# Optimization experiments

Hardware: AMD Instinct MI355X
Metric: run time of the kernel (lower is better)

## Reference

```python
import jax, jax.numpy as jnp
import numpy as np


def gin_layer(x, src, dst, ew, w1, b1, w2, b2):
    # message: gather source features, scale by edge weight  [E, d]
    msg = x[src] * ew[:, None]
    # scatter-add into destination nodes  [N, d]
    agg = jax.ops.segment_sum(msg, dst, num_segments=x.shape[0])
    # GIN update: (1 + eps) * x + aggregate, eps = 0 (default)
    h = agg + x
    # 2-layer MLP (Linear -> ReLU -> Linear, plain last layer)
    h = jax.nn.relu(h @ w1 + b1)
    return h @ w2 + b2


def setup_inputs() -> dict:
    key = jax.random.key(0)
    ks = jax.random.split(key, 16)
    N, E, D = 100000, 1000000, 64
    x = jax.random.normal(ks[0], (N, D), dtype=jnp.float32)
    edge_index = jax.random.randint(ks[1], (2, E), 0, N)
    edge_weight = jax.random.uniform(ks[2], (E,), dtype=jnp.float32)

    def lin(k, fi, fo):
        return jax.random.normal(k, (fi, fo), dtype=jnp.float32) * (1.0 / np.sqrt(fi))

    return {
        "x": x, "edge_index": edge_index, "edge_weight": edge_weight,
        "w11": lin(ks[3], 64, 64),  "b11": jnp.zeros(64, jnp.float32),
        "w12": lin(ks[4], 64, 64),  "b12": jnp.zeros(64, jnp.float32),
        "w21": lin(ks[5], 64, 128), "b21": jnp.zeros(128, jnp.float32),
        "w22": lin(ks[6], 128, 64), "b22": jnp.zeros(64, jnp.float32),
        "w31": lin(ks[7], 64, 64),  "b31": jnp.zeros(64, jnp.float32),
        "w32": lin(ks[8], 64, 64),  "b32": jnp.zeros(64, jnp.float32),
    }


def reference(x, edge_index, edge_weight,
              w11, b11, w12, b12,
              w21, b21, w22, b22,
              w31, b31, w32, b32):
    src, dst = edge_index[0], edge_index[1]
    # dropout is identity in eval mode
    h = gin_layer(x, src, dst, edge_weight, w11, b11, w12, b12)
    h = jax.nn.relu(h)
    h = gin_layer(h, src, dst, edge_weight, w21, b21, w22, b22)
    h = jax.nn.relu(h)
    h = gin_layer(h, src, dst, edge_weight, w31, b31, w32, b32)
    return h
```

## Files before the change

### kernel.cpp

```cpp
#include <hip/hip_runtime.h>
#include <math.h>


#define FEAT  64
#define BINW  128
#define BSH   7
#define NBLK  256
#define SRCB  25

typedef __attribute__((ext_vector_type(8))) short bfrag;
typedef __attribute__((ext_vector_type(4))) float ffrag;

__device__ __forceinline__ unsigned short f2bf_rne(float x) {
    union { float f; unsigned u; } v; v.f = x;
    unsigned r = (v.u + 0x7fffu + ((v.u >> 16) & 1u)) >> 16;
    return (unsigned short)r;
}
__device__ __forceinline__ float bf2f(unsigned short h) {
    union { unsigned u; float f; } v; v.u = ((unsigned)h) << 16;
    return v.f;
}

__device__ __forceinline__ void pack_one(const float* __restrict__ w,
                                         unsigned short* __restrict__ hi,
                                         unsigned short* __restrict__ lo,
                                         int K, int Hc, int i) {
    int KF = K >> 5;
    int j    = i & 7;
    int lane = (i >> 3) & 63;
    int fb   = i >> 9;
    int kf   = fb % KF;
    int cg   = fb / KF;
    int k    = kf * 32 + ((lane >> 4) << 3) + j;
    int col  = cg * 16 + (lane & 15);
    float x = w[k * Hc + col];
    unsigned short h = f2bf_rne(x);
    hi[i] = h;
    lo[i] = f2bf_rne(x - bf2f(h));
}

__global__ __launch_bounds__(256)
void k_pre(const float4* __restrict__ x4, ushort4* __restrict__ xb4,
           int n4, int gCvt,
           const int* __restrict__ dst, int* __restrict__ counts,
           int E, int NBINS,
           const float* w11, const float* w12, const float* w21,
           const float* w22, const float* w31, const float* w32,
           unsigned short* p11h, unsigned short* p11l,
           unsigned short* p12h, unsigned short* p12l,
           unsigned short* p21h, unsigned short* p21l,
           unsigned short* p22h, unsigned short* p22l,
           unsigned short* p31h, unsigned short* p31l,
           unsigned short* p32h, unsigned short* p32l) {
    __shared__ int h[1024];
    const int bb = blockIdx.x, tid = threadIdx.x;
    if (bb < gCvt) {
        int i = bb * 256 + tid;
        if (i < n4) {
            float4 v = x4[i];
            ushort4 o;
            o.x = f2bf_rne(v.x); o.y = f2bf_rne(v.y);
            o.z = f2bf_rne(v.z); o.w = f2bf_rne(v.w);
            xb4[i] = o;
        }
    } else if (bb < gCvt + NBLK) {
        const int b = bb - gCvt;
        for (int i = tid; i < NBINS; i += 256) h[i] = 0;
        __syncthreads();
        const int chunk = (E + NBLK - 1) / NBLK;
        const int ebeg = b * chunk;
        const int eend = (ebeg + chunk < E) ? ebeg + chunk : E;
        for (int e = ebeg + tid; e < eend; e += 256)
            atomicAdd(&h[dst[e] >> BSH], 1);
        __syncthreads();
        for (int i = tid; i < NBINS; i += 256)
            counts[i * NBLK + b] = h[i];
    } else {
        int i = (bb - gCvt - NBLK) * 256 + tid;
        if      (i <  4096) pack_one(w11, p11h, p11l,  64,  64, i);
        else if (i <  8192) pack_one(w12, p12h, p12l,  64,  64, i - 4096);
        else if (i < 16384) pack_one(w21, p21h, p21l,  64, 128, i - 8192);
        else if (i < 24576) pack_one(w22, p22h, p22l, 128,  64, i - 16384);
        else if (i < 28672) pack_one(w31, p31h, p31l,  64,  64, i - 24576);
        else                pack_one(w32, p32h, p32l,  64,  64, i - 28672);
    }
}

__global__ __launch_bounds__(256)
void k_scanA2(int* __restrict__ counts, int* __restrict__ bintotal,
              int* __restrict__ rowptr, int NBINS, int N, int E) {
    __shared__ int tmp[256];
    const int bin = blockIdx.x, tid = threadIdx.x;
    int c = counts[bin * NBLK + tid];
    tmp[tid] = c;
    __syncthreads();
    for (int off = 1; off < 256; off <<= 1) {
        int t = (tid >= off) ? tmp[tid - off] : 0;
        __syncthreads();
        tmp[tid] += t;
        __syncthreads();
    }
    counts[bin * NBLK + tid] = tmp[tid] - c;
    if (tid == 255) bintotal[bin] = tmp[255];
    if (bin == 0 && tid == 0) rowptr[N] = E;
}

__global__ __launch_bounds__(256)
void k_place2(const int* __restrict__ src, const int* __restrict__ dst,
              const float* __restrict__ ew, const int* __restrict__ counts,
              const int* __restrict__ bintotal, int* __restrict__ binstart,
              int2* __restrict__ binbuf, int E, int NBINS) {
    __shared__ int bs[1024];
    __shared__ int tmp[256];
    __shared__ int base[1024];
    const int b = blockIdx.x, tid = threadIdx.x;

    int v[4]; int s = 0;
#pragma unroll
    for (int j = 0; j < 4; ++j) {
        int idx = tid * 4 + j;
        v[j] = (idx < NBINS) ? bintotal[idx] : 0;
        s += v[j];
    }
    tmp[tid] = s;
    __syncthreads();
    for (int off = 1; off < 256; off <<= 1) {
        int t = (tid >= off) ? tmp[tid - off] : 0;
        __syncthreads();
        tmp[tid] += t;
        __syncthreads();
    }
    int run = tmp[tid] - s;
#pragma unroll
    for (int j = 0; j < 4; ++j) {
        bs[tid * 4 + j] = run;
        run += v[j];
    }
    __syncthreads();

    if (b == 0) {
        for (int i = tid; i < NBINS; i += 256) binstart[i] = bs[i];
        if (tid == 0) binstart[NBINS] = E;
    }

    for (int i = tid; i < NBINS; i += 256)
        base[i] = bs[i] + counts[i * NBLK + b];
    __syncthreads();

    const int chunk = (E + NBLK - 1) / NBLK;
    const int ebeg = b * chunk;
    const int eend = (ebeg + chunk < E) ? ebeg + chunk : E;
    for (int e = ebeg + tid; e < eend; e += 256) {
        int d = dst[e];
        int slot = atomicAdd(&base[d >> BSH], 1);
        int key = ((d & (BINW - 1)) << SRCB) | src[e];
        binbuf[slot] = make_int2(key, __float_as_int(ew[e]));
    }
}

__global__ __launch_bounds__(256)
void k_binsort(const int2* __restrict__ binbuf, const int* __restrict__ binstart,
               int* __restrict__ rowptr, int2* __restrict__ csr, int N) {
    __shared__ int cnt[BINW];
    __shared__ int cur[BINW];
    const int b    = blockIdx.x;
    const int base = binstart[b];
    const int ne   = binstart[b + 1] - base;
    const int tid  = threadIdx.x;

    if (tid < BINW) cnt[tid] = 0;
    __syncthreads();
    for (int i = tid; i < ne; i += 256)
        atomicAdd(&cnt[(binbuf[base + i].x >> SRCB) & (BINW - 1)], 1);
    __syncthreads();
    if (tid < BINW) cur[tid] = cnt[tid];
    __syncthreads();
    for (int off = 1; off < BINW; off <<= 1) {
        int v = (tid < BINW && tid >= off) ? cur[tid - off] : 0;
        __syncthreads();
        if (tid < BINW) cur[tid] += v;
        __syncthreads();
    }
    if (tid < BINW) {
        int ex = cur[tid] - cnt[tid];
        int node = b * BINW + tid;
        if (node < N) rowptr[node] = base + ex;
        cur[tid] = ex;
    }
    __syncthreads();
    for (int i = tid; i < ne; i += 256) {
        int2 e = binbuf[base + i];
        int dl = (e.x >> SRCB) & (BINW - 1);
        int r = atomicAdd(&cur[dl], 1);
        csr[base + r] = make_int2(e.x & ((1 << SRCB) - 1), e.y);
    }
}

template<int H, bool RELU_OUT, bool OUT_BF16>
__global__ __launch_bounds__(256)
void k_fused(const ushort* __restrict__ in, void* __restrict__ outv,
             const int* __restrict__ rowptr, const int2* __restrict__ csr,
             const unsigned short* __restrict__ w1h, const unsigned short* __restrict__ w1l,
             const float* __restrict__ b1,
             const unsigned short* __restrict__ w2h, const unsigned short* __restrict__ w2l,
             const float* __restrict__ b2, int N, int E) {
    constexpr int SH   = H + 4;
    constexpr int CG1  = H / 16;
    constexpr int CGH1 = CG1 / 4;
    constexpr int KF2  = H / 32;
    __shared__ float hs[16 * SH];

    const int t = threadIdx.x;
    const int wk = t >> 6, lane = t & 63;
    const int m = lane & 15, q = lane >> 4;
    const int tnode0 = blockIdx.x * 16;
    float* hw = hs;
    const ushort4* in4 = reinterpret_cast<const ushort4*>(in);

    int rp_l = 0;
    {
        int idx = tnode0 + wk * 4 + lane;
        if (lane <= 4) rp_l = rowptr[idx <= N ? idx : N];
    }

    int gnode = tnode0 + wk * 4 + q;
    int gnodeC = gnode < N ? gnode : N - 1;
    ushort4 xr = in4[(size_t)gnodeC * 16 + m];

    {
        const int nl  = wk * 4 + q;
        const int beg = __shfl(rp_l, q);
        const int end = __shfl(rp_l, q + 1);
        float4 acc = make_float4(0.f, 0.f, 0.f, 0.f);
        for (int p = beg; p < end; p += 16) {
            int   s[16];
            float w[16];
#pragma unroll
            for (int u = 0; u < 16; ++u) {
                int i = p + u;
                int2 ev = csr[i < E ? i : E - 1];
                s[u] = ev.x;
                w[u] = (i < end) ? __int_as_float(ev.y) : 0.f;
            }
            ushort4 v4[16];
#pragma unroll
            for (int u = 0; u < 16; ++u)
                v4[u] = in4[(unsigned)s[u] * 16u + m];
#pragma unroll
            for (int u = 0; u < 16; ++u) {
                acc.x = fmaf(w[u], bf2f(v4[u].x), acc.x);
                acc.y = fmaf(w[u], bf2f(v4[u].y), acc.y);
                acc.z = fmaf(w[u], bf2f(v4[u].z), acc.z);
                acc.w = fmaf(w[u], bf2f(v4[u].w), acc.w);
            }
        }
        acc.x += bf2f(xr.x); acc.y += bf2f(xr.y);
        acc.z += bf2f(xr.z); acc.w += bf2f(xr.w);
        *reinterpret_cast<float4*>(&hw[nl * SH + m * 4]) = acc;
    }
    __syncthreads();

    const bfrag* w1hp = reinterpret_cast<const bfrag*>(w1h);
    const bfrag* w1lp = reinterpret_cast<const bfrag*>(w1l);
    const bfrag* w2hp = reinterpret_cast<const bfrag*>(w2h);
    const bfrag* w2lp = reinterpret_cast<const bfrag*>(w2l);

    bfrag ah[2], al[2];
#pragma unroll
    for (int kf = 0; kf < 2; ++kf) {
        const float* base = &hw[m * SH + kf * 32 + q * 8];
        float4 u0 = *reinterpret_cast<const float4*>(base);
        float4 u1 = *reinterpret_cast<const float4*>(base + 4);
        float u[8] = {u0.x, u0.y, u0.z, u0.w, u1.x, u1.y, u1.z, u1.w};
#pragma unroll
        for (int j = 0; j < 8; ++j) {
            unsigned short hb = f2bf_rne(u[j]);
            ah[kf][j] = (short)hb;
            al[kf][j] = (short)f2bf_rne(u[j] - bf2f(hb));
        }
    }
    __syncthreads();

#pragma unroll
    for (int cgi = 0; cgi < CGH1; ++cgi) {
        const int cg = wk * CGH1 + cgi;
        ffrag c = {0.f, 0.f, 0.f, 0.f};
#pragma unroll
        for (int kf = 0; kf < 2; ++kf) {
            bfrag bh = w1hp[(cg * 2 + kf) * 64 + lane];
            bfrag bl = w1lp[(cg * 2 + kf) * 64 + lane];
            c = __builtin_amdgcn_mfma_f32_16x16x32_bf16(ah[kf], bh, c, 0, 0, 0);
            c = __builtin_amdgcn_mfma_f32_16x16x32_bf16(al[kf], bh, c, 0, 0, 0);
            c = __builtin_amdgcn_mfma_f32_16x16x32_bf16(ah[kf], bl, c, 0, 0, 0);
        }
        float bias = b1[cg * 16 + m];
#pragma unroll
        for (int r = 0; r < 4; ++r) {
            float hv = fmaxf(c[r] + bias, 0.f);
            hw[(q * 4 + r) * SH + cg * 16 + m] = hv;
        }
    }
    __syncthreads();

    bfrag gh[KF2], gl[KF2];
#pragma unroll
    for (int kf = 0; kf < KF2; ++kf) {
        const float* base = &hw[m * SH + kf * 32 + q * 8];
        float4 u0 = *reinterpret_cast<const float4*>(base);
        float4 u1 = *reinterpret_cast<const float4*>(base + 4);
        float u[8] = {u0.x, u0.y, u0.z, u0.w, u1.x, u1.y, u1.z, u1.w};
#pragma unroll
        for (int j = 0; j < 8; ++j) {
            unsigned short hb = f2bf_rne(u[j]);
            gh[kf][j] = (short)hb;
            gl[kf][j] = (short)f2bf_rne(u[j] - bf2f(hb));
        }
    }

    {
        const int cg = wk;
        ffrag c = {0.f, 0.f, 0.f, 0.f};
#pragma unroll
        for (int kf = 0; kf < KF2; ++kf) {
            bfrag bh = w2hp[(cg * KF2 + kf) * 64 + lane];
            bfrag bl = w2lp[(cg * KF2 + kf) * 64 + lane];
            c = __builtin_amdgcn_mfma_f32_16x16x32_bf16(gh[kf], bh, c, 0, 0, 0);
            c = __builtin_amdgcn_mfma_f32_16x16x32_bf16(gl[kf], bh, c, 0, 0, 0);
            c = __builtin_amdgcn_mfma_f32_16x16x32_bf16(gh[kf], bl, c, 0, 0, 0);
        }
        float bias = b2[cg * 16 + m];
#pragma unroll
        for (int r = 0; r < 4; ++r) {
            int nd = tnode0 + q * 4 + r;
            if (nd < N) {
                float v = c[r] + bias;
                if (RELU_OUT) v = fmaxf(v, 0.f);
                if (OUT_BF16)
                    ((unsigned short*)outv)[(size_t)nd * FEAT + cg * 16 + m] = f2bf_rne(v);
                else
                    ((float*)outv)[(size_t)nd * FEAT + cg * 16 + m] = v;
            }
        }
    }
}

extern "C" void kernel_launch(void* const* d_in, const int* in_sizes, int n_in,
                              void* d_out, int out_size, void* d_ws, size_t ws_size,
                              hipStream_t stream) {
    const float* x   = (const float*)d_in[0];
    const int*   ei  = (const int*)  d_in[1];
    const float* ew  = (const float*)d_in[2];
    const float* w11 = (const float*)d_in[3];
    const float* b11 = (const float*)d_in[4];
    const float* w12 = (const float*)d_in[5];
    const float* b12 = (const float*)d_in[6];
    const float* w21 = (const float*)d_in[7];
    const float* b21 = (const float*)d_in[8];
    const float* w22 = (const float*)d_in[9];
    const float* b22 = (const float*)d_in[10];
    const float* w31 = (const float*)d_in[11];
    const float* b31 = (const float*)d_in[12];
    const float* w32 = (const float*)d_in[13];
    const float* b32 = (const float*)d_in[14];

    const int N = in_sizes[0] / FEAT;
    const int E = in_sizes[2];
    const int* srci = ei;
    const int* dsti = ei + E;
    const int NBINS = (N + BINW - 1) >> BSH;

    unsigned short* xb0 = (unsigned short*)d_ws;
    unsigned short* xb1 = xb0 + (size_t)N * FEAT;
    int*   rowptr   = (int*)(xb1 + (size_t)N * FEAT);
    int*   counts   = rowptr + (N + 1);
    int*   bintotal = counts + NBINS * NBLK;
    int*   binstart = bintotal + NBINS;
    size_t a16 = ((size_t)(binstart + NBINS + 1) + 15) & ~(size_t)15;
    int2*  binbuf   = (int2*)a16;
    int2*  csr      = (int2*)(binbuf + E);
    size_t pk = (size_t)(csr + E);
    unsigned short* p11h = (unsigned short*)pk;
    unsigned short* p11l = p11h + 4096;
    unsigned short* p12h = p11l + 4096;
    unsigned short* p12l = p12h + 4096;
    unsigned short* p21h = p12l + 4096;
    unsigned short* p21l = p21h + 8192;
    unsigned short* p22h = p21l + 8192;
    unsigned short* p22l = p22h + 8192;
    unsigned short* p31h = p22l + 8192;
    unsigned short* p31l = p31h + 4096;
    unsigned short* p32h = p31l + 4096;
    unsigned short* p32l = p32h + 4096;
    float* outF = (float*)d_out;

    const int n4   = N * 16;
    const int gCvt = (n4 + 255) / 256;
    const int gMlp = (N + 15) / 16;
    const int gPre = gCvt + NBLK + 128;

    k_pre<<<gPre, 256, 0, stream>>>((const float4*)x, (ushort4*)xb0, n4, gCvt,
                                    dsti, counts, E, NBINS,
                                    w11, w12, w21, w22, w31, w32,
                                    p11h, p11l, p12h, p12l, p21h, p21l,
                                    p22h, p22l, p31h, p31l, p32h, p32l);
    k_scanA2 <<<NBINS, 256, 0, stream>>>(counts, bintotal, rowptr, NBINS, N, E);
    k_place2 <<<NBLK,  256, 0, stream>>>(srci, dsti, ew, counts, bintotal,
                                         binstart, binbuf, E, NBINS);
    k_binsort<<<NBINS, 256, 0, stream>>>(binbuf, binstart, rowptr, csr, N);

    k_fused<64,  true,  true ><<<gMlp, 256, 0, stream>>>(xb0, xb1, rowptr, csr,
                                                         p11h, p11l, b11, p12h, p12l, b12, N, E);
    k_fused<128, true,  true ><<<gMlp, 256, 0, stream>>>(xb1, xb0, rowptr, csr,
                                                         p21h, p21l, b21, p22h, p22l, b22, N, E);
    k_fused<64,  false, false><<<gMlp, 256, 0, stream>>>(xb0, outF, rowptr, csr,
                                                         p31h, p31l, b31, p32h, p32l, b32, N, E);
}
```

Baseline: 274.4 us.

## Pad per-node CSR segments to 16 edges and load edges as int4 pairs

```diff
diff --git a/kernel.cpp b/kernel.cpp
--- a/kernel.cpp
+++ b/kernel.cpp
@@ -7,6 +7,7 @@
 #define BSH   7
 #define NBLK  256
 #define SRCB  25
+#define PADSLACK 2048
 
 typedef __attribute__((ext_vector_type(8))) short bfrag;
 typedef __attribute__((ext_vector_type(4))) float ffrag;
@@ -87,8 +88,7 @@
 }
 
 __global__ __launch_bounds__(256)
-void k_scanA2(int* __restrict__ counts, int* __restrict__ bintotal,
-              int* __restrict__ rowptr, int NBINS, int N, int E) {
+void k_scanA2(int* __restrict__ counts, int* __restrict__ bintotal, int NBINS) {
     __shared__ int tmp[256];
     const int bin = blockIdx.x, tid = threadIdx.x;
     int c = counts[bin * NBLK + tid];
@@ -102,7 +102,6 @@
     }
     counts[bin * NBLK + tid] = tmp[tid] - c;
     if (tid == 255) bintotal[bin] = tmp[255];
-    if (bin == 0 && tid == 0) rowptr[N] = E;
 }
 
 __global__ __launch_bounds__(256)
@@ -160,20 +159,24 @@
 
 __global__ __launch_bounds__(256)
 void k_binsort(const int2* __restrict__ binbuf, const int* __restrict__ binstart,
-               int* __restrict__ rowptr, int2* __restrict__ csr, int N) {
+               int* __restrict__ pbeg, int* __restrict__ pend,
+               int2* __restrict__ csr_pad, int N) {
     __shared__ int cnt[BINW];
     __shared__ int cur[BINW];
+    __shared__ int pex[BINW];
     const int b    = blockIdx.x;
     const int base = binstart[b];
     const int ne   = binstart[b + 1] - base;
     const int tid  = threadIdx.x;
+    const int base_pad = ((base + 15) & ~15) + b * PADSLACK;
 
     if (tid < BINW) cnt[tid] = 0;
     __syncthreads();
     for (int i = tid; i < ne; i += 256)
         atomicAdd(&cnt[(binbuf[base + i].x >> SRCB) & (BINW - 1)], 1);
     __syncthreads();
-    if (tid < BINW) cur[tid] = cnt[tid];
+    int pc = 0;
+    if (tid < BINW) { pc = (cnt[tid] + 15) & ~15; cur[tid] = pc; }
     __syncthreads();
     for (int off = 1; off < BINW; off <<= 1) {
         int v = (tid < BINW && tid >= off) ? cur[tid - off] : 0;
@@ -182,28 +185,41 @@
         __syncthreads();
     }
     if (tid < BINW) {
-        int ex = cur[tid] - cnt[tid];
+        int ex = cur[tid] - pc;
+        pex[tid] = ex;
         int node = b * BINW + tid;
-        if (node < N) rowptr[node] = base + ex;
-        cur[tid] = ex;
+        if (node < N) {
+            pbeg[node] = base_pad + ex;
+            pend[node] = base_pad + ex + pc;
+        }
+        cur[tid] = 0;
     }
     __syncthreads();
     for (int i = tid; i < ne; i += 256) {
         int2 e = binbuf[base + i];
         int dl = (e.x >> SRCB) & (BINW - 1);
         int r = atomicAdd(&cur[dl], 1);
-        csr[base + r] = make_int2(e.x & ((1 << SRCB) - 1), e.y);
+        csr_pad[base_pad + pex[dl] + r] = make_int2(e.x & ((1 << SRCB) - 1), e.y);
+    }
+    __syncthreads();
+    if (tid < BINW) {
+        int c = cnt[tid];
+        int pcn = (c + 15) & ~15;
+        int o = base_pad + pex[tid];
+        for (int j = c; j < pcn; ++j)
+            csr_pad[o + j] = make_int2(0, 0);
     }
 }
 
 template<int H, bool RELU_OUT, bool OUT_BF16>
 __global__ __launch_bounds__(256)
 void k_fused(const ushort* __restrict__ in, void* __restrict__ outv,
-             const int* __restrict__ rowptr, const int2* __restrict__ csr,
+             const int* __restrict__ pbeg, const int* __restrict__ pend,
+             const int2* __restrict__ csr_pad,
              const unsigned short* __restrict__ w1h, const unsigned short* __restrict__ w1l,
              const float* __restrict__ b1,
              const unsigned short* __restrict__ w2h, const unsigned short* __restrict__ w2l,
-             const float* __restrict__ b2, int N, int E) {
+             const float* __restrict__ b2, int N) {
     constexpr int SH   = H + 4;
     constexpr int CG1  = H / 16;
     constexpr int CGH1 = CG1 / 4;
@@ -216,42 +232,39 @@
     const int tnode0 = blockIdx.x * 16;
     float* hw = hs;
     const ushort4* in4 = reinterpret_cast<const ushort4*>(in);
-
-    int rp_l = 0;
+    const int4* csr4 = reinterpret_cast<const int4*>(csr_pad);
+
+    const int gnode = tnode0 + wk * 4 + q;
+    const int beg = pbeg[gnode];
+    const int end = pend[gnode];
+    ushort4 xr = in4[(size_t)gnode * 16 + m];
+
     {
-        int idx = tnode0 + wk * 4 + lane;
-        if (lane <= 4) rp_l = rowptr[idx <= N ? idx : N];
-    }
-
-    int gnode = tnode0 + wk * 4 + q;
-    int gnodeC = gnode < N ? gnode : N - 1;
-    ushort4 xr = in4[(size_t)gnodeC * 16 + m];
-
-    {
-        const int nl  = wk * 4 + q;
-        const int beg = __shfl(rp_l, q);
-        const int end = __shfl(rp_l, q + 1);
+        const int nl = wk * 4 + q;
         float4 acc = make_float4(0.f, 0.f, 0.f, 0.f);
         for (int p = beg; p < end; p += 16) {
-            int   s[16];
-            float w[16];
-#pragma unroll
-            for (int u = 0; u < 16; ++u) {
-                int i = p + u;
-                int2 ev = csr[i < E ? i : E - 1];
-                s[u] = ev.x;
-                w[u] = (i < end) ? __int_as_float(ev.y) : 0.f;
+            int4 e2[8];
+#pragma unroll
+            for (int u = 0; u < 8; ++u)
+                e2[u] = csr4[(p >> 1) + u];
+            ushort4 v4[16];
+#pragma unroll
+            for (int u = 0; u < 8; ++u) {
+                v4[2*u]   = in4[(unsigned)e2[u].x * 16u + m];
+                v4[2*u+1] = in4[(unsigned)e2[u].z * 16u + m];
             }
-            ushort4 v4[16];
-#pragma unroll
-            for (int u = 0; u < 16; ++u)
-                v4[u] = in4[(unsigned)s[u] * 16u + m];
-#pragma unroll
-            for (int u = 0; u < 16; ++u) {
-                acc.x = fmaf(w[u], bf2f(v4[u].x), acc.x);
-                acc.y = fmaf(w[u], bf2f(v4[u].y), acc.y);
-                acc.z = fmaf(w[u], bf2f(v4[u].z), acc.z);
-                acc.w = fmaf(w[u], bf2f(v4[u].w), acc.w);
+#pragma unroll
+            for (int u = 0; u < 8; ++u) {
+                float w0 = __int_as_float(e2[u].y);
+                float w1 = __int_as_float(e2[u].w);
+                acc.x = fmaf(w0, bf2f(v4[2*u].x), acc.x);
+                acc.y = fmaf(w0, bf2f(v4[2*u].y), acc.y);
+                acc.z = fmaf(w0, bf2f(v4[2*u].z), acc.z);
+                acc.w = fmaf(w0, bf2f(v4[2*u].w), acc.w);
+                acc.x = fmaf(w1, bf2f(v4[2*u+1].x), acc.x);
+                acc.y = fmaf(w1, bf2f(v4[2*u+1].y), acc.y);
+                acc.z = fmaf(w1, bf2f(v4[2*u+1].z), acc.z);
+                acc.w = fmaf(w1, bf2f(v4[2*u+1].w), acc.w);
             }
         }
         acc.x += bf2f(xr.x); acc.y += bf2f(xr.y);
@@ -281,6 +294,7 @@
     }
     __syncthreads();
 
+    __builtin_amdgcn_s_setprio(1);
 #pragma unroll
     for (int cgi = 0; cgi < CGH1; ++cgi) {
         const int cg = wk * CGH1 + cgi;
@@ -300,6 +314,7 @@
             hw[(q * 4 + r) * SH + cg * 16 + m] = hv;
         }
     }
+    __builtin_amdgcn_s_setprio(0);
     __syncthreads();
 
     bfrag gh[KF2], gl[KF2];
@@ -320,6 +335,7 @@
     {
         const int cg = wk;
         ffrag c = {0.f, 0.f, 0.f, 0.f};
+        __builtin_amdgcn_s_setprio(1);
 #pragma unroll
         for (int kf = 0; kf < KF2; ++kf) {
             bfrag bh = w2hp[(cg * KF2 + kf) * 64 + lane];
@@ -328,6 +344,7 @@
             c = __builtin_amdgcn_mfma_f32_16x16x32_bf16(gl[kf], bh, c, 0, 0, 0);
             c = __builtin_amdgcn_mfma_f32_16x16x32_bf16(gh[kf], bl, c, 0, 0, 0);
         }
+        __builtin_amdgcn_s_setprio(0);
         float bias = b2[cg * 16 + m];
 #pragma unroll
         for (int r = 0; r < 4; ++r) {
@@ -371,14 +388,15 @@
 
     unsigned short* xb0 = (unsigned short*)d_ws;
     unsigned short* xb1 = xb0 + (size_t)N * FEAT;
-    int*   rowptr   = (int*)(xb1 + (size_t)N * FEAT);
-    int*   counts   = rowptr + (N + 1);
+    int*   pbeg     = (int*)(xb1 + (size_t)N * FEAT);
+    int*   pend     = pbeg + N;
+    int*   counts   = pend + N;
     int*   bintotal = counts + NBINS * NBLK;
     int*   binstart = bintotal + NBINS;
     size_t a16 = ((size_t)(binstart + NBINS + 1) + 15) & ~(size_t)15;
     int2*  binbuf   = (int2*)a16;
-    int2*  csr      = (int2*)(binbuf + E);
-    size_t pk = (size_t)(csr + E);
+    int2*  csr_pad  = (int2*)(binbuf + E);
+    size_t pk = (size_t)(csr_pad + E + (size_t)NBINS * PADSLACK + 16);
     unsigned short* p11h = (unsigned short*)pk;
     unsigned short* p11l = p11h + 4096;
     unsigned short* p12h = p11l + 4096;
@@ -403,15 +421,16 @@
                                     w11, w12, w21, w22, w31, w32,
                                     p11h, p11l, p12h, p12l, p21h, p21l,
                                     p22h, p22l, p31h, p31l, p32h, p32l);
-    k_scanA2 <<<NBINS, 256, 0, stream>>>(counts, bintotal, rowptr, NBINS, N, E);
+    k_scanA2 <<<NBINS, 256, 0, stream>>>(counts, bintotal, NBINS);
     k_place2 <<<NBLK,  256, 0, stream>>>(srci, dsti, ew, counts, bintotal,
                                          binstart, binbuf, E, NBINS);
-    k_binsort<<<NBINS, 256, 0, stream>>>(binbuf, binstart, rowptr, csr, N);
-
-    k_fused<64,  true,  true ><<<gMlp, 256, 0, stream>>>(xb0, xb1, rowptr, csr,
-                                                         p11h, p11l, b11, p12h, p12l, b12, N, E);
-    k_fused<128, true,  true ><<<gMlp, 256, 0, stream>>>(xb1, xb0, rowptr, csr,
-                                                         p21h, p21l, b21, p22h, p22l, b22, N, E);
-    k_fused<64,  false, false><<<gMlp, 256, 0, stream>>>(xb0, outF, rowptr, csr,
-                                                         p31h, p31l, b31, p32h, p32l, b32, N, E);
-}
+    k_binsort<<<NBINS, 256, 0, stream>>>(binbuf, binstart, pbeg, pend,
+                                         csr_pad, N);
+
+    k_fused<64,  true,  true ><<<gMlp, 256, 0, stream>>>(xb0, xb1, pbeg, pend, csr_pad,
+                                                         p11h, p11l, b11, p12h, p12l, b12, N);
+    k_fused<128, true,  true ><<<gMlp, 256, 0, stream>>>(xb1, xb0, pbeg, pend, csr_pad,
+                                                         p21h, p21l, b21, p22h, p22l, b22, N);
+    k_fused<64,  false, false><<<gMlp, 256, 0, stream>>>(xb0, outF, pbeg, pend, csr_pad,
+                                                         p31h, p31l, b31, p32h, p32l, b32, N);
+}
```

Result: faster. 263.1 us (-4.1%).
